# Optimization experiments

Measured on AMD Instinct MI355X. Metric: run time of the kernel, lower is better.

Reference implementation:

```python
import jax, jax.numpy as jnp
import numpy as np
from jax import lax

# NOTE: ResidualConvBlock and SS2DChanelFirst are reconstructed from the repo's
# conventions: ResidualConvBlock = act(conv3x3 -> act -> conv3x3 + 1x1 skip);
# SS2DChanelFirst = standard VMamba SS2D (in_proj -> dw-conv3x3 -> SiLU ->
# 4-direction cross-scan selective scan -> cross-merge -> LayerNorm -> *SiLU(z)
# gate -> out_proj) operating on NCHW tensors.

B, CIN, H, W = 4, 6, 64, 64
DM, DI, K, N, R, NL, GROUPS = 72, 144, 4, 8, 4, 2, 12


def conv2d(x, w, b=None, groups=1):
    out = lax.conv_general_dilated(x, w, (1, 1), 'SAME',
                                   dimension_numbers=('NCHW', 'OIHW', 'NCHW'),
                                   feature_group_count=groups)
    if b is not None:
        out = out + b[None, :, None, None]
    return out


def lrelu(x, s):
    return jnp.where(x >= 0, x, s * x)


def selective_scan(u, delta, A, Bs, Cs, D):
    # u, delta: (b,K,C,L); A: (K,C,N); Bs, Cs: (b,K,N,L); D: (K,C)
    b, k, c, l = u.shape
    n = A.shape[-1]
    ul = jnp.moveaxis(u, -1, 0)
    dl = jnp.moveaxis(delta, -1, 0)
    Bl = jnp.moveaxis(Bs, -1, 0)
    Cl = jnp.moveaxis(Cs, -1, 0)
    h0 = jnp.zeros((b, k, c, n), u.dtype)

    def step(h, xt):
        d_t, u_t, B_t, C_t = xt
        h = h * jnp.exp(d_t[..., None] * A) + (d_t * u_t)[..., None] * B_t[:, :, None, :]
        return h, jnp.einsum('bkcn,bkn->bkc', h, C_t)

    _, ys = lax.scan(step, h0, (dl, ul, Bl, Cl))
    return jnp.moveaxis(ys, 0, -1) + u * D[None, :, :, None]


def ss2d(x, in_w, dw_w, dw_b, xp_w, dtp_w, dtp_b, A_logs, Ds, ong, onb, op_w):
    b, dm, h_, w_ = x.shape
    l = h_ * w_
    xz = jnp.einsum('ec,bchw->behw', in_w, x)  # (b, 2*DI, h, w)
    xi, z = xz[:, :DI], xz[:, DI:]
    xi = jax.nn.silu(conv2d(xi, dw_w, dw_b, groups=DI))
    # cross-scan: row-major, col-major, and their reverses
    x0 = xi.reshape(b, DI, l)
    x1 = jnp.swapaxes(xi, 2, 3).reshape(b, DI, l)
    xs = jnp.stack([x0, x1, x0[..., ::-1], x1[..., ::-1]], axis=1)  # (b,4,DI,l)
    x_dbl = jnp.einsum('bkdl,kcd->bkcl', xs, xp_w)  # (b,4,R+2N,l)
    dts, Bs, Cs = x_dbl[:, :, :R], x_dbl[:, :, R:R + N], x_dbl[:, :, R + N:]
    dts = jnp.einsum('bkrl,kdr->bkdl', dts, dtp_w)
    delta = jax.nn.softplus(dts + dtp_b[None, :, :, None])
    A = -jnp.exp(A_logs).reshape(K, DI, N)
    ys = selective_scan(xs, delta, A, Bs, Cs, Ds.reshape(K, DI))  # (b,4,DI,l)
    # cross-merge
    y = ys[:, 0] + ys[:, 2, :, ::-1]
    yt = ys[:, 1] + ys[:, 3, :, ::-1]
    y = y + jnp.swapaxes(yt.reshape(b, DI, w_, h_), 2, 3).reshape(b, DI, l)
    y = jnp.swapaxes(y, 1, 2)  # (b,l,DI)
    mu = y.mean(-1, keepdims=True)
    var = ((y - mu) ** 2).mean(-1, keepdims=True)
    y = (y - mu) / jnp.sqrt(var + 1e-5) * ong + onb
    y = y * jax.nn.silu(jnp.swapaxes(z.reshape(b, DI, l), 1, 2))
    out = jnp.einsum('bld,ed->ble', y, op_w)  # (b,l,DM)
    return jnp.swapaxes(out, 1, 2).reshape(b, dm, h_, w_)


def groupnorm(x, g, bta, groups):
    b, c, h_, w_ = x.shape
    xg = x.reshape(b, groups, c // groups, h_ * w_)
    mu = xg.mean((2, 3), keepdims=True)
    var = ((xg - mu) ** 2).mean((2, 3), keepdims=True)
    xg = (xg - mu) / jnp.sqrt(var + 1e-5)
    return xg.reshape(b, c, h_, w_) * g[None, :, None, None] + bta[None, :, None, None]


def setup_inputs() -> dict:
    key = jax.random.key(0)
    ks = iter(jax.random.split(key, 32))
    nrm = lambda shp, s=0.05: jax.random.normal(next(ks), shp, jnp.float32) * s
    inp = {
        'image': jax.random.normal(next(ks), (B, CIN, H, W), jnp.float32),
        'cb_w1': nrm((DM, CIN, 3, 3), 0.1), 'cb_b1': nrm((DM,), 0.02),
        'cb_w2': nrm((DM, DM, 3, 3), 0.05), 'cb_b2': nrm((DM,), 0.02),
        'cb_ws': nrm((DM, CIN, 1, 1), 0.1), 'cb_bs': nrm((DM,), 0.02),
        'in_w': nrm((NL, 2 * DI, DM), 0.05),
        'dw_w': nrm((NL, DI, 1, 3, 3), 0.1), 'dw_b': nrm((NL, DI), 0.02),
        'xp_w': nrm((NL, K, R + 2 * N, DI), 0.05),
        'dtp_w': nrm((NL, K, DI, R), 0.1), 'dtp_b': nrm((NL, K, DI), 0.1),
        'A_logs': nrm((NL, K * DI, N), 0.5),
        'Ds': jnp.ones((NL, K * DI), jnp.float32) + nrm((NL, K * DI), 0.05),
        'ong': jnp.ones((NL, DI), jnp.float32), 'onb': jnp.zeros((NL, DI), jnp.float32),
        'op_w': nrm((NL, DM, DI), 0.05),
        'gn_g': jnp.ones((NL, DM), jnp.float32), 'gn_b': jnp.zeros((NL, DM), jnp.float32),
        'l1_w': nrm((NL, DM, DM), 0.1), 'l1_b': nrm((NL, DM), 0.02),
        'l2_w': nrm((NL, DM, DM), 0.1), 'l2_b': nrm((NL, DM), 0.02),
        'shrink_w': nrm((CIN, DM, 3, 3), 0.05), 'shrink_b': nrm((CIN,), 0.02),
    }
    return inp


def reference(image, cb_w1, cb_b1, cb_w2, cb_b2, cb_ws, cb_bs, in_w, dw_w, dw_b,
              xp_w, dtp_w, dtp_b, A_logs, Ds, ong, onb, op_w, gn_g, gn_b,
              l1_w, l1_b, l2_w, l2_b, shrink_w, shrink_b):
    # ResidualConvBlock (expand 6 -> 72), leaky_relu
    h = lrelu(conv2d(image, cb_w1, cb_b1), 0.01)
    h = conv2d(h, cb_w2, cb_b2) + conv2d(image, cb_ws, cb_bs)
    x = lrelu(h, 0.01)
    for i in range(NL):
        x = ss2d(x, in_w[i], dw_w[i], dw_b[i], xp_w[i], dtp_w[i], dtp_b[i],
                 A_logs[i], Ds[i], ong[i], onb[i], op_w[i])
        x = groupnorm(x, gn_g[i], gn_b[i], GROUPS)
        x = jnp.einsum('oc,bchw->bohw', l1_w[i], x) + l1_b[i][None, :, None, None]
        x = lrelu(x, 0.04)
        x = jnp.einsum('oc,bchw->bohw', l2_w[i], x) + l2_b[i][None, :, None, None]
    x = conv2d(x, shrink_w, shrink_b)
    return jax.nn.sigmoid(x)
```

## Files before the change

kernel.cpp:

```cpp
#include <hip/hip_runtime.h>
#include <math.h>

#define BB 4
#define CI 6
#define LL 4096
#define DMC 72
#define DIC 144
#define KD 4
#define NS 8
#define RD 4
#define NLAYER 2
#define GRP 12
#define NCH 128
#define TS 32
#define PP 4356
#define L2E 1.4426950408889634f

__device__ __forceinline__ float sigmoidf_(float x){ return 1.f/(1.f+__expf(-x)); }
__device__ __forceinline__ float siluf_(float x){ return x*sigmoidf_(x); }
__device__ __forceinline__ float softplusf_(float x){
  return fmaxf(x,0.f) + __logf(1.f + __expf(-fabsf(x)));
}

__device__ __forceinline__ int padidx(int p){ return 66*(p>>6) + (p&63) + 67; }

__device__ __forceinline__ int dirmap(int k, int l){
  switch(k & 3){
    case 0: return l;
    case 1: return ((l & 63) << 6) | (l >> 6);
    case 2: return (LL-1) - l;
    default: { int m = (LL-1) - l; return ((m & 63) << 6) | (m >> 6); }
  }
}

#define LOAD9(ip, a) do { \
  a[0]=(ip)[-67]; a[1]=(ip)[-66]; a[2]=(ip)[-65]; \
  a[3]=(ip)[-1];  a[4]=(ip)[0];   a[5]=(ip)[1];   \
  a[6]=(ip)[65];  a[7]=(ip)[66];  a[8]=(ip)[67];  } while(0)

__global__ void k_halo(float* __restrict__ pads, int nplanes){
  int plane = blockIdx.x;
  if (plane >= nplanes) return;
  int t = threadIdx.x;
  if (t >= 260) return;
  float* pl = pads + (size_t)plane*PP;
  int off;
  if (t < 132){
    int row = (t < 66) ? 0 : 65;
    int col = (t < 66) ? t : t-66;
    off = row*66 + col;
  } else {
    int j = t - 132;
    int col = (j < 64) ? 0 : 65;
    int row = 1 + (j & 63);
    off = row*66 + col;
  }
  pl[off] = 0.f;
}

__global__ void k_pad_img(const float* __restrict__ img, float* __restrict__ img_pad){
  int idx = blockIdx.x*256 + threadIdx.x;
  if (idx >= BB*CI*LL) return;
  int p = idx & 4095; int bc = idx >> 12;
  img_pad[(size_t)bc*PP + padidx(p)] = img[idx];
}

__global__ void k_conv1(const float* __restrict__ img_pad, const float* __restrict__ w,
                        const float* __restrict__ bias, float* __restrict__ tmp_pad){
  int bid = blockIdx.x;
  int t = bid & 15; int r = bid >> 4; int o = r % DMC; int b = r / DMC;
  int p = t*256 + threadIdx.x;
  int pb = padidx(p);
  float acc = bias[o];
  const float* wb = w + o*CI*9;
  #pragma unroll
  for (int ic=0; ic<CI; ++ic){
    const float* ip = img_pad + (size_t)(b*CI+ic)*PP + pb;
    float a[9]; LOAD9(ip, a);
    #pragma unroll
    for (int q=0;q<9;++q) acc += a[q]*wb[ic*9+q];
  }
  tmp_pad[(size_t)(b*DMC+o)*PP + pb] = acc >= 0.f ? acc : 0.01f*acc;
}

__global__ void k_conv2init(const float* __restrict__ img, const float* __restrict__ b2,
                            const float* __restrict__ wsc, const float* __restrict__ bsc,
                            float* __restrict__ xout){
  int bid = blockIdx.x;
  int t = bid & 15; int r = bid >> 4; int og = r % 18; int b = r / 18;
  int p = t*256 + threadIdx.x;
  float acc[4];
  #pragma unroll
  for (int j=0;j<4;++j) acc[j] = b2[og*4+j] + bsc[og*4+j];
  #pragma unroll
  for (int ic=0; ic<CI; ++ic){
    float v = img[((b*CI+ic)<<12)+p];
    #pragma unroll
    for (int j=0;j<4;++j) acc[j] += v * wsc[(og*4+j)*CI+ic];
  }
  #pragma unroll
  for (int j=0;j<4;++j)
    xout[((b*DMC+og*4+j)<<12)+p] = acc[j];
}

__global__ void k_conv2(const float* __restrict__ tmp_pad,
                        const float* __restrict__ w2, float* __restrict__ xout){
  int bid = blockIdx.x;
  int t = bid & 15; int r = bid >> 4; int og = r % 18; r /= 18;
  int icg = r & 1; int b = r >> 1;
  int p = t*256 + threadIdx.x;
  int pb = padidx(p);
  float acc[4] = {0.f,0.f,0.f,0.f};
  const float* ipb = tmp_pad + (size_t)b*DMC*PP + pb;
  const float* wb  = w2 + (size_t)(og*4)*DMC*9;
  #pragma unroll 2
  for (int ii=0; ii<36; ++ii){
    int ic = icg*36 + ii;
    const float* ip = ipb + (size_t)ic*PP;
    float a[9]; LOAD9(ip, a);
    const float* wp = wb + ic*9;
    #pragma unroll
    for (int j=0;j<4;++j){
      float s = 0.f;
      #pragma unroll
      for (int q=0;q<9;++q) s += a[q]*wp[(size_t)j*DMC*9 + q];
      acc[j] += s;
    }
  }
  #pragma unroll
  for (int j=0;j<4;++j)
    atomicAdd(xout + ((b*DMC+og*4+j)<<12)+p, acc[j]);
}

__global__ void k_xz(const float* __restrict__ x, const float* __restrict__ inw,
                     float* __restrict__ xz_pad, float* __restrict__ z_t, int relu){
  int bid = blockIdx.x;
  int t = bid & 15; int r = bid >> 4; int eg = r % 36; int b = r / 36;
  int p = t*256 + threadIdx.x;
  float acc[8] = {0.f,0.f,0.f,0.f,0.f,0.f,0.f,0.f};
  for (int c0=0; c0<DMC; c0+=4){
    float a[4];
    #pragma unroll
    for (int q=0;q<4;++q) a[q] = x[((b*DMC+c0+q)<<12)+p];
    if (relu){
      #pragma unroll
      for (int q=0;q<4;++q) a[q] = a[q] >= 0.f ? a[q] : 0.01f*a[q];
    }
    #pragma unroll
    for (int j=0;j<8;++j){
      float4 w = *(const float4*)(inw + (eg*8+j)*DMC + c0);
      acc[j] += a[0]*w.x + a[1]*w.y + a[2]*w.z + a[3]*w.w;
    }
  }
  if (eg < 18){
    int pb = padidx(p);
    #pragma unroll
    for (int j=0;j<8;++j) xz_pad[(size_t)(b*DIC+eg*8+j)*PP + pb] = acc[j];
  } else {
    float* zb = z_t + ((size_t)b*LL+p)*DIC + (eg*8-DIC);
    *(float4*)(zb)   = make_float4(acc[0],acc[1],acc[2],acc[3]);
    *(float4*)(zb+4) = make_float4(acc[4],acc[5],acc[6],acc[7]);
  }
}

__global__ void k_dw(const float* __restrict__ xz_pad, const float* __restrict__ dww,
                     const float* __restrict__ dwb, float* __restrict__ xi_t){
  int bid = blockIdx.x;
  int t = bid & 15; int r = bid >> 4; int c = r % DIC; int b = r / DIC;
  int p = t*256 + threadIdx.x;
  int pb = padidx(p);
  const float* ip = xz_pad + (size_t)(b*DIC+c)*PP + pb;
  const float* wp = dww + c*9;
  float a[9]; LOAD9(ip, a);
  float acc = dwb[c];
  #pragma unroll
  for (int q=0;q<9;++q) acc += a[q]*wp[q];
  xi_t[((size_t)b*LL+p)*DIC + c] = siluf_(acc);
}

__global__ void k_xdbl(const float* __restrict__ xi_t, const float* __restrict__ xpw,
                       float* __restrict__ xdbl){
  int bid = blockIdx.x;
  int t = bid & 15; int r = bid >> 4;
  int kk = r & 3; r >>= 2; int part = r % 10; int b = r / 10;
  int p = t*256 + threadIdx.x;
  const float* xib = xi_t + ((size_t)b*LL + p)*DIC;
  const float* wk = xpw + (size_t)(kk*20 + part*2)*DIC;
  float acc[2] = {0.f,0.f};
  for (int d=0; d<DIC; d+=4){
    float4 v = *(const float4*)(xib + d);
    #pragma unroll
    for (int c=0;c<2;++c){
      float4 w = *(const float4*)(wk + (size_t)c*DIC + d);
      acc[c] += v.x*w.x + v.y*w.y + v.z*w.z + v.w*w.w;
    }
  }
  float* dst = xdbl + ((size_t)(b*KD+kk)*LL + p)*20 + part*2;
  dst[0] = acc[0]; dst[1] = acc[1];
}

__device__ __forceinline__ void scan_decode(int idx, int& b, int& k, int& ch, int& c){
  c = idx % DIC;
  int r = idx / DIC;
  ch = r % NCH;
  r /= NCH;
  k = r & 3; b = r >> 2;
}

__global__ void k_p1(const float* __restrict__ xi_t, const float* __restrict__ xdbl,
                     const float* __restrict__ dtpw, const float* __restrict__ dtpb,
                     const float* __restrict__ alog,
                     float* __restrict__ cumA, float* __restrict__ hp){
  int idx = blockIdx.x*256 + threadIdx.x;
  if (idx >= BB*KD*NCH*DIC) return;
  int b,k,ch,c; scan_decode(idx,b,k,ch,c);
  float Arow[NS];
  #pragma unroll
  for (int n=0;n<NS;++n) Arow[n] = -__expf(alog[(k*DIC+c)*NS+n]) * L2E;
  float4 wdt = *(const float4*)(dtpw + (k*DIC+c)*RD);
  float bdt = dtpb[k*DIC+c];
  const float* xd = xdbl + (size_t)(b*KD+k)*LL*20;
  const float* xib = xi_t + (size_t)b*LL*DIC + c;
  float h[NS];
  #pragma unroll
  for (int n=0;n<NS;++n) h[n]=0.f;
  float sumd = 0.f;
  #pragma unroll 2
  for (int t=0; t<TS; ++t){
    int l = ch*TS + t;
    int ps = dirmap(k,l);
    const float* row = xd + (size_t)ps*20;
    float4 q0 = *(const float4*)(row);
    float4 q1 = *(const float4*)(row+4);
    float4 q2 = *(const float4*)(row+8);
    float u = xib[(size_t)ps*DIC];
    float dt = bdt + q0.x*wdt.x + q0.y*wdt.y + q0.z*wdt.z + q0.w*wdt.w;
    dt = softplusf_(dt);
    sumd += dt;
    float du = dt*u;
    float Bv[NS] = {q1.x,q1.y,q1.z,q1.w,q2.x,q2.y,q2.z,q2.w};
    #pragma unroll
    for (int n=0;n<NS;++n)
      h[n] = h[n]*exp2f(dt*Arow[n]) + du*Bv[n];
  }
  size_t base = ((size_t)((b*KD+k)*NCH + ch)*NS)*DIC + c;
  #pragma unroll
  for (int n=0;n<NS;++n) hp[base + n*DIC] = h[n];
  #pragma unroll
  for (int n=0;n<NS;++n) cumA[base + n*DIC] = exp2f(sumd*Arow[n]);
}

__global__ void k_p2(const float* __restrict__ cumA, float* __restrict__ hp){
  int idx = blockIdx.x*256 + threadIdx.x;
  if (idx >= BB*KD*NS*DIC) return;
  int c = idx % DIC; int n = (idx/DIC) % NS; int bk = idx/(DIC*NS);
  float h = 0.f;
  #pragma unroll 4
  for (int ch=0; ch<NCH; ++ch){
    size_t base = ((size_t)(bk*NCH+ch)*NS + n)*DIC + c;
    float a = cumA[base];
    float pp = hp[base];
    hp[base] = h;
    h = a*h + pp;
  }
}

__global__ void k_p3(const float* __restrict__ xi_t, const float* __restrict__ xdbl,
                     const float* __restrict__ dtpw, const float* __restrict__ dtpb,
                     const float* __restrict__ alog, const float* __restrict__ Dsv,
                     const float* __restrict__ hin, float* __restrict__ y_t){
  int idx = blockIdx.x*256 + threadIdx.x;
  if (idx >= BB*KD*NCH*DIC) return;
  int b,k,ch,c; scan_decode(idx,b,k,ch,c);
  float Arow[NS];
  #pragma unroll
  for (int n=0;n<NS;++n) Arow[n] = -__expf(alog[(k*DIC+c)*NS+n]) * L2E;
  float4 wdt = *(const float4*)(dtpw + (k*DIC+c)*RD);
  float bdt = dtpb[k*DIC+c];
  float Dv = Dsv[k*DIC+c];
  const float* xd = xdbl + (size_t)(b*KD+k)*LL*20;
  const float* xib = xi_t + (size_t)b*LL*DIC + c;
  float* yb = y_t + (size_t)b*LL*DIC + c;
  float h[NS];
  size_t base = ((size_t)((b*KD+k)*NCH + ch)*NS)*DIC + c;
  #pragma unroll
  for (int n=0;n<NS;++n) h[n] = hin[base + n*DIC];
  #pragma unroll 2
  for (int t=0; t<TS; ++t){
    int l = ch*TS + t;
    int ps = dirmap(k,l);
    const float* row = xd + (size_t)ps*20;
    float4 q0 = *(const float4*)(row);
    float4 q1 = *(const float4*)(row+4);
    float4 q2 = *(const float4*)(row+8);
    float4 q3 = *(const float4*)(row+12);
    float4 q4 = *(const float4*)(row+16);
    float u = xib[(size_t)ps*DIC];
    float dt = bdt + q0.x*wdt.x + q0.y*wdt.y + q0.z*wdt.z + q0.w*wdt.w;
    dt = softplusf_(dt);
    float du = dt*u;
    float Bv[NS] = {q1.x,q1.y,q1.z,q1.w,q2.x,q2.y,q2.z,q2.w};
    float Cv[NS] = {q3.x,q3.y,q3.z,q3.w,q4.x,q4.y,q4.z,q4.w};
    float y = 0.f;
    #pragma unroll
    for (int n=0;n<NS;++n){
      h[n] = h[n]*exp2f(dt*Arow[n]) + du*Bv[n];
      y += h[n]*Cv[n];
    }
    y += u*Dv;
    atomicAdd(yb + (size_t)ps*DIC, y);
  }
}

__global__ void k_oproj(const float* __restrict__ y_t, const float* __restrict__ z_t,
                        const float* __restrict__ ong, const float* __restrict__ onb,
                        const float* __restrict__ opw, float* __restrict__ xout){
  __shared__ float ly[DIC*65];
  __shared__ float red1[8][64], red2[8][64];
  __shared__ float lmu[64], lrs[64];
  int bid = blockIdx.x;
  int tile = bid & 63; int b = bid >> 6;
  int pstart = tile*64;
  const float* src = y_t + ((size_t)b*LL + pstart)*DIC;
  for (int i = threadIdx.x; i < 64*DIC; i += 512){
    int px = i / DIC; int d = i - px*DIC;
    ly[d*65 + px] = src[i];
  }
  __syncthreads();
  int px = threadIdx.x & 63;
  int grp = threadIdx.x >> 6;
  {
    float s=0.f, q=0.f;
    for (int d=grp*18; d<grp*18+18; ++d){
      float v = ly[d*65+px]; s += v; q += v*v;
    }
    red1[grp][px]=s; red2[grp][px]=q;
  }
  __syncthreads();
  if (grp == 0){
    float st=0.f, qt=0.f;
    #pragma unroll
    for (int g=0;g<8;++g){ st += red1[g][px]; qt += red2[g][px]; }
    float mu = st*(1.f/DIC);
    float var = qt*(1.f/DIC) - mu*mu;
    lmu[px] = mu;
    lrs[px] = rsqrtf(var + 1e-5f);
  }
  __syncthreads();
  const float* zsrc = z_t + ((size_t)b*LL + pstart)*DIC;
  for (int i = threadIdx.x; i < 64*DIC; i += 512){
    int ppx = i / DIC; int d = i - ppx*DIC;
    float zv = zsrc[i];
    float v = ly[d*65+ppx];
    ly[d*65+ppx] = ((v - lmu[ppx])*lrs[ppx]*ong[d] + onb[d]) * siluf_(zv);
  }
  __syncthreads();
  int ocg = __builtin_amdgcn_readfirstlane(grp);
  float acc[9];
  #pragma unroll
  for (int j=0;j<9;++j) acc[j]=0.f;
  const float* wb = opw + (size_t)ocg*9*DIC;
  #pragma unroll 4
  for (int d=0; d<DIC; ++d){
    float a = ly[d*65 + px];
    #pragma unroll
    for (int j=0;j<9;++j) acc[j] += a * wb[(size_t)j*DIC + d];
  }
  #pragma unroll
  for (int j=0;j<9;++j)
    xout[((size_t)(b*DMC + ocg*9 + j)<<12) + pstart + px] = acc[j];
}

__global__ void k_gnA(const float* __restrict__ x, float* __restrict__ stats){
  __shared__ float s1[256], s2[256];
  int bid = blockIdx.x;
  int t = bid & 15; int r = bid >> 4; int gr = r % GRP; int b = r / GRP;
  float ls=0.f, lq=0.f;
  #pragma unroll
  for (int it=0; it<6; ++it){
    int i = t*1536 + it*256 + threadIdx.x;
    int c = gr*6 + (i>>12); int p = i & 4095;
    float v = x[((size_t)(b*DMC+c)<<12)+p];
    ls += v; lq += v*v;
  }
  s1[threadIdx.x]=ls; s2[threadIdx.x]=lq; __syncthreads();
  for (int s=128; s>0; s>>=1){
    if (threadIdx.x < s){ s1[threadIdx.x]+=s1[threadIdx.x+s]; s2[threadIdx.x]+=s2[threadIdx.x+s]; }
    __syncthreads();
  }
  if (threadIdx.x == 0){
    atomicAdd(stats + (b*GRP+gr)*2,     s1[0]);
    atomicAdd(stats + (b*GRP+gr)*2 + 1, s2[0]);
  }
}

__global__ void k_gnAB(const float* __restrict__ stats, const float* __restrict__ g,
                       const float* __restrict__ bta, float* __restrict__ gnab){
  int idx = blockIdx.x*256 + threadIdx.x;
  if (idx >= BB*DMC) return;
  int c = idx % DMC; int b = idx / DMC; int gr = c / 6;
  float s = stats[(b*GRP+gr)*2];
  float q = stats[(b*GRP+gr)*2 + 1];
  const float inv = 1.f/(6.f*LL);
  float mu = s*inv;
  float var = q*inv - mu*mu;
  float rs = rsqrtf(var + 1e-5f);
  float A = rs*g[c];
  gnab[idx] = A;
  gnab[BB*DMC + idx] = bta[c] - mu*A;
}

__global__ void k_dense1(const float* __restrict__ xin, const float* __restrict__ gnab,
                         const float* __restrict__ w, const float* __restrict__ bias,
                         float* __restrict__ xout){
  int bid = blockIdx.x;
  int t = bid & 15; int r = bid >> 4; int eg = r % 36; int b = r / 36;
  int p = t*256 + threadIdx.x;
  float acc[2] = { bias[eg*2], bias[eg*2+1] };
  const float* Aab = gnab + b*DMC;
  const float* Bab = gnab + BB*DMC + b*DMC;
  for (int c0=0; c0<DMC; c0+=4){
    float a[4];
    #pragma unroll
    for (int q=0;q<4;++q){
      float v = xin[((size_t)(b*DMC+c0+q)<<12)+p];
      a[q] = v*Aab[c0+q] + Bab[c0+q];
    }
    #pragma unroll
    for (int j=0;j<2;++j){
      float4 w0 = *(const float4*)(w + (eg*2+j)*DMC + c0);
      acc[j] += a[0]*w0.x + a[1]*w0.y + a[2]*w0.z + a[3]*w0.w;
    }
  }
  #pragma unroll
  for (int j=0;j<2;++j)
    xout[((size_t)(b*DMC+eg*2+j)<<12)+p] = acc[j];
}

__global__ void k_dense2(const float* __restrict__ xin, const float* __restrict__ w,
                         const float* __restrict__ bias, float* __restrict__ xout,
                         float* __restrict__ pad_out){
  int bid = blockIdx.x;
  int t = bid & 15; int r = bid >> 4; int eg = r % 36; int b = r / 36;
  int p = t*256 + threadIdx.x;
  float acc[2] = { bias[eg*2], bias[eg*2+1] };
  for (int c0=0; c0<DMC; c0+=4){
    float a[4];
    #pragma unroll
    for (int q=0;q<4;++q){
      float v = xin[((size_t)(b*DMC+c0+q)<<12)+p];
      a[q] = v >= 0.f ? v : 0.04f*v;
    }
    #pragma unroll
    for (int j=0;j<2;++j){
      float4 w0 = *(const float4*)(w + (eg*2+j)*DMC + c0);
      acc[j] += a[0]*w0.x + a[1]*w0.y + a[2]*w0.z + a[3]*w0.w;
    }
  }
  #pragma unroll
  for (int j=0;j<2;++j){
    xout[((size_t)(b*DMC+eg*2+j)<<12)+p] = acc[j];
    if (pad_out) pad_out[(size_t)(b*DMC+eg*2+j)*PP + padidx(p)] = acc[j];
  }
}

__global__ void k_shrinkA(const float* __restrict__ x_pad, const float* __restrict__ w,
                          float* __restrict__ pacc){
  int bid = blockIdx.x;
  int t = bid & 15; int r = bid >> 4; int icg = r % 24; int b = r / 24;
  int p = t*256 + threadIdx.x;
  int pb = padidx(p);
  float acc[6] = {0.f,0.f,0.f,0.f,0.f,0.f};
  const float* ipb = x_pad + (size_t)b*DMC*PP + pb;
  #pragma unroll
  for (int ii=0; ii<3; ++ii){
    int ic = icg*3 + ii;
    const float* ip = ipb + (size_t)ic*PP;
    float a[9]; LOAD9(ip, a);
    #pragma unroll
    for (int o=0;o<6;++o){
      const float* wp = w + (o*DMC+ic)*9;
      float s = 0.f;
      #pragma unroll
      for (int q=0;q<9;++q) s += a[q]*wp[q];
      acc[o] += s;
    }
  }
  #pragma unroll
  for (int o=0;o<6;++o)
    atomicAdd(pacc + ((size_t)(b*CI+o)<<12)+p, acc[o]);
}

__global__ void k_sig(const float* __restrict__ pacc, const float* __restrict__ bias,
                      float* __restrict__ out){
  int idx = blockIdx.x*256 + threadIdx.x;
  if (idx >= BB*CI*LL) return;
  int o = (idx>>12) % CI;
  out[idx] = sigmoidf_(pacc[idx] + bias[o]);
}

extern "C" void kernel_launch(void* const* d_in, const int* in_sizes, int n_in,
                              void* d_out, int out_size, void* d_ws, size_t ws_size,
                              hipStream_t stream){
  const float* image = (const float*)d_in[0];
  const float* cb_w1 = (const float*)d_in[1];
  const float* cb_b1 = (const float*)d_in[2];
  const float* cb_w2 = (const float*)d_in[3];
  const float* cb_b2 = (const float*)d_in[4];
  const float* cb_ws = (const float*)d_in[5];
  const float* cb_bs = (const float*)d_in[6];
  const float* in_w  = (const float*)d_in[7];
  const float* dw_w  = (const float*)d_in[8];
  const float* dw_b  = (const float*)d_in[9];
  const float* xp_w  = (const float*)d_in[10];
  const float* dtp_w = (const float*)d_in[11];
  const float* dtp_b = (const float*)d_in[12];
  const float* A_logs= (const float*)d_in[13];
  const float* Ds    = (const float*)d_in[14];
  const float* ong   = (const float*)d_in[15];
  const float* onb   = (const float*)d_in[16];
  const float* op_w  = (const float*)d_in[17];
  const float* gn_g  = (const float*)d_in[18];
  const float* gn_b  = (const float*)d_in[19];
  const float* l1_w  = (const float*)d_in[20];
  const float* l1_b  = (const float*)d_in[21];
  const float* l2_w  = (const float*)d_in[22];
  const float* l2_b  = (const float*)d_in[23];
  const float* sh_w  = (const float*)d_in[24];
  const float* sh_b  = (const float*)d_in[25];

  const size_t SZ_X  = (size_t)BB*DMC*LL;
  const size_t SZ_C  = (size_t)BB*DIC*LL;
  const size_t SZ_XD = (size_t)BB*KD*20*LL;
  const size_t SZ_IP = (size_t)BB*CI*PP;
  const size_t SZ_TP = (size_t)BB*DMC*PP;
  const size_t SZ_ZP = (size_t)BB*DIC*PP;

  float* ws = (float*)d_ws;
  size_t off = 0;
  float* x     = ws + off; off += SZ_X;
  float* tmp   = ws + off; off += SZ_X;
  float* z_t   = ws + off; off += SZ_C;
  float* xi_t  = ws + off; off += SZ_C;
  float* xdbl  = ws + off; off += SZ_XD;
  float* cumA  = ws + off; off += SZ_C;
  float* hp    = ws + off; off += SZ_C;
  float* pads  = ws + off;
  float* img_pad = pads;
  float* tmp_pad = img_pad + SZ_IP;
  float* xz_pad  = tmp_pad + SZ_TP;
  off += SZ_IP + SZ_TP + SZ_ZP;
  float* gnstats = ws + off; off += 2*BB*GRP;
  float* gnab    = ws + off; off += 2*BB*DMC;
  if (ws_size < off*sizeof(float)) return;
  float* y_t = cumA;

  dim3 blk(256);
  const int NPLANES = BB*CI + BB*DMC + BB*DIC;

  k_halo<<<dim3(NPLANES), blk, 0, stream>>>(pads, NPLANES);
  k_pad_img<<<dim3(BB*CI*16), blk, 0, stream>>>(image, img_pad);
  k_conv1<<<dim3(BB*DMC*16), blk, 0, stream>>>(img_pad, cb_w1, cb_b1, tmp_pad);
  k_conv2init<<<dim3(BB*18*16), blk, 0, stream>>>(image, cb_b2, cb_ws, cb_bs, x);
  k_conv2<<<dim3(BB*2*18*16), blk, 0, stream>>>(tmp_pad, cb_w2, x);

  for (int i=0; i<NLAYER; ++i){
    const float* in_w_i  = in_w  + (size_t)i*2*DIC*DMC;
    const float* dw_w_i  = dw_w  + (size_t)i*DIC*9;
    const float* dw_b_i  = dw_b  + (size_t)i*DIC;
    const float* xp_w_i  = xp_w  + (size_t)i*KD*20*DIC;
    const float* dtp_w_i = dtp_w + (size_t)i*KD*DIC*RD;
    const float* dtp_b_i = dtp_b + (size_t)i*KD*DIC;
    const float* alog_i  = A_logs+ (size_t)i*KD*DIC*NS;
    const float* Ds_i    = Ds    + (size_t)i*KD*DIC;
    const float* ong_i   = ong   + (size_t)i*DIC;
    const float* onb_i   = onb   + (size_t)i*DIC;
    const float* op_w_i  = op_w  + (size_t)i*DMC*DIC;
    const float* gn_g_i  = gn_g  + (size_t)i*DMC;
    const float* gn_b_i  = gn_b  + (size_t)i*DMC;
    const float* l1_w_i  = l1_w  + (size_t)i*DMC*DMC;
    const float* l1_b_i  = l1_b  + (size_t)i*DMC;
    const float* l2_w_i  = l2_w  + (size_t)i*DMC*DMC;
    const float* l2_b_i  = l2_b  + (size_t)i*DMC;

    k_xz  <<<dim3(BB*36*16), blk, 0, stream>>>(x, in_w_i, xz_pad, z_t, (i==0)?1:0);
    k_dw  <<<dim3(BB*DIC*16), blk, 0, stream>>>(xz_pad, dw_w_i, dw_b_i, xi_t);
    k_xdbl<<<dim3(BB*10*KD*16), blk, 0, stream>>>(xi_t, xp_w_i, xdbl);
    k_p1  <<<dim3(BB*KD*NCH*DIC/256), blk, 0, stream>>>(xi_t, xdbl, dtp_w_i, dtp_b_i, alog_i, cumA, hp);
    k_p2  <<<dim3(BB*KD*NS*DIC/256), blk, 0, stream>>>(cumA, hp);
    hipMemsetAsync(y_t, 0, SZ_C*sizeof(float), stream);
    k_p3  <<<dim3(BB*KD*NCH*DIC/256), blk, 0, stream>>>(xi_t, xdbl, dtp_w_i, dtp_b_i, alog_i, Ds_i, hp, y_t);
    k_oproj<<<dim3(BB*64), dim3(512), 0, stream>>>(y_t, z_t, ong_i, onb_i, op_w_i, x);
    hipMemsetAsync(gnstats, 0, 2*BB*GRP*sizeof(float), stream);
    k_gnA <<<dim3(BB*GRP*16), blk, 0, stream>>>(x, gnstats);
    k_gnAB<<<dim3(2), blk, 0, stream>>>(gnstats, gn_g_i, gn_b_i, gnab);
    k_dense1<<<dim3(BB*36*16), blk, 0, stream>>>(x, gnab, l1_w_i, l1_b_i, tmp);
    k_dense2<<<dim3(BB*36*16), blk, 0, stream>>>(tmp, l2_w_i, l2_b_i, x,
                                                 (i==NLAYER-1) ? tmp_pad : (float*)nullptr);
  }

  hipMemsetAsync(tmp, 0, (size_t)BB*CI*LL*sizeof(float), stream);
  k_shrinkA<<<dim3(BB*24*16), blk, 0, stream>>>(tmp_pad, sh_w, tmp);
  k_sig<<<dim3((BB*CI*LL+255)/256), blk, 0, stream>>>(tmp, sh_b, (float*)d_out);
}
```

Measured before the change: 538.8 us.

## Double scan chunk count, widen per-thread outputs, and fold memsets into kernels

The chunked selective scan now uses 256 chunks of 16 steps instead of 128 of 32, with deeper unrolling, to expose more parallel threads in the first and third scan passes. The x_dbl projection and both dense 1x1 layers compute more output channels per thread, cutting the number of blocks and the repeated input reads. The two memsets are removed: the second scan pass zeroes the cumA buffer that is reused as y_t, and the output-projection kernel zeroes the group-norm stats. The scan carry buffers grow to match the larger chunk count, and the extra chunks make the sequential second pass longer.

```diff
diff --git a/kernel.cpp b/kernel.cpp
--- a/kernel.cpp
+++ b/kernel.cpp
@@ -11,8 +11,8 @@
 #define RD 4
 #define NLAYER 2
 #define GRP 12
-#define NCH 128
-#define TS 32
+#define NCH 256
+#define TS 16
 #define PP 4356
 #define L2E 1.4426950408889634f
 
@@ -182,21 +182,22 @@
                        float* __restrict__ xdbl){
   int bid = blockIdx.x;
   int t = bid & 15; int r = bid >> 4;
-  int kk = r & 3; r >>= 2; int part = r % 10; int b = r / 10;
+  int kk = r & 3; r >>= 2; int part = r & 3; int b = r >> 2;
   int p = t*256 + threadIdx.x;
   const float* xib = xi_t + ((size_t)b*LL + p)*DIC;
-  const float* wk = xpw + (size_t)(kk*20 + part*2)*DIC;
-  float acc[2] = {0.f,0.f};
+  const float* wk = xpw + (size_t)(kk*20 + part*5)*DIC;
+  float acc[5] = {0.f,0.f,0.f,0.f,0.f};
   for (int d=0; d<DIC; d+=4){
     float4 v = *(const float4*)(xib + d);
     #pragma unroll
-    for (int c=0;c<2;++c){
+    for (int c=0;c<5;++c){
       float4 w = *(const float4*)(wk + (size_t)c*DIC + d);
       acc[c] += v.x*w.x + v.y*w.y + v.z*w.z + v.w*w.w;
     }
   }
-  float* dst = xdbl + ((size_t)(b*KD+kk)*LL + p)*20 + part*2;
-  dst[0] = acc[0]; dst[1] = acc[1];
+  float* dst = xdbl + ((size_t)(b*KD+kk)*LL + p)*20 + part*5;
+  #pragma unroll
+  for (int c=0;c<5;++c) dst[c] = acc[c];
 }
 
 __device__ __forceinline__ void scan_decode(int idx, int& b, int& k, int& ch, int& c){
@@ -225,7 +226,7 @@
   #pragma unroll
   for (int n=0;n<NS;++n) h[n]=0.f;
   float sumd = 0.f;
-  #pragma unroll 2
+  #pragma unroll 4
   for (int t=0; t<TS; ++t){
     int l = ch*TS + t;
     int ps = dirmap(k,l);
@@ -250,7 +251,7 @@
   for (int n=0;n<NS;++n) cumA[base + n*DIC] = exp2f(sumd*Arow[n]);
 }
 
-__global__ void k_p2(const float* __restrict__ cumA, float* __restrict__ hp){
+__global__ void k_p2(float* __restrict__ cumA, float* __restrict__ hp){
   int idx = blockIdx.x*256 + threadIdx.x;
   if (idx >= BB*KD*NS*DIC) return;
   int c = idx % DIC; int n = (idx/DIC) % NS; int bk = idx/(DIC*NS);
@@ -260,6 +261,7 @@
     size_t base = ((size_t)(bk*NCH+ch)*NS + n)*DIC + c;
     float a = cumA[base];
     float pp = hp[base];
+    cumA[base] = 0.f;
     hp[base] = h;
     h = a*h + pp;
   }
@@ -285,7 +287,7 @@
   size_t base = ((size_t)((b*KD+k)*NCH + ch)*NS)*DIC + c;
   #pragma unroll
   for (int n=0;n<NS;++n) h[n] = hin[base + n*DIC];
-  #pragma unroll 2
+  #pragma unroll 4
   for (int t=0; t<TS; ++t){
     int l = ch*TS + t;
     int ps = dirmap(k,l);
@@ -314,11 +316,13 @@
 
 __global__ void k_oproj(const float* __restrict__ y_t, const float* __restrict__ z_t,
                         const float* __restrict__ ong, const float* __restrict__ onb,
-                        const float* __restrict__ opw, float* __restrict__ xout){
+                        const float* __restrict__ opw, float* __restrict__ xout,
+                        float* __restrict__ gnstats){
   __shared__ float ly[DIC*65];
   __shared__ float red1[8][64], red2[8][64];
   __shared__ float lmu[64], lrs[64];
   int bid = blockIdx.x;
+  if (bid == 0 && threadIdx.x < 2*BB*GRP) gnstats[threadIdx.x] = 0.f;
   int tile = bid & 63; int b = bid >> 6;
   int pstart = tile*64;
   const float* src = y_t + ((size_t)b*LL + pstart)*DIC;
@@ -414,9 +418,11 @@
                          const float* __restrict__ w, const float* __restrict__ bias,
                          float* __restrict__ xout){
   int bid = blockIdx.x;
-  int t = bid & 15; int r = bid >> 4; int eg = r % 36; int b = r / 36;
-  int p = t*256 + threadIdx.x;
-  float acc[2] = { bias[eg*2], bias[eg*2+1] };
+  int t = bid & 15; int r = bid >> 4; int eg = r % 18; int b = r / 18;
+  int p = t*256 + threadIdx.x;
+  float acc[4];
+  #pragma unroll
+  for (int j=0;j<4;++j) acc[j] = bias[eg*4+j];
   const float* Aab = gnab + b*DMC;
   const float* Bab = gnab + BB*DMC + b*DMC;
   for (int c0=0; c0<DMC; c0+=4){
@@ -427,23 +433,25 @@
       a[q] = v*Aab[c0+q] + Bab[c0+q];
     }
     #pragma unroll
-    for (int j=0;j<2;++j){
-      float4 w0 = *(const float4*)(w + (eg*2+j)*DMC + c0);
+    for (int j=0;j<4;++j){
+      float4 w0 = *(const float4*)(w + (eg*4+j)*DMC + c0);
       acc[j] += a[0]*w0.x + a[1]*w0.y + a[2]*w0.z + a[3]*w0.w;
     }
   }
   #pragma unroll
-  for (int j=0;j<2;++j)
-    xout[((size_t)(b*DMC+eg*2+j)<<12)+p] = acc[j];
+  for (int j=0;j<4;++j)
+    xout[((size_t)(b*DMC+eg*4+j)<<12)+p] = acc[j];
 }
 
 __global__ void k_dense2(const float* __restrict__ xin, const float* __restrict__ w,
                          const float* __restrict__ bias, float* __restrict__ xout,
                          float* __restrict__ pad_out){
   int bid = blockIdx.x;
-  int t = bid & 15; int r = bid >> 4; int eg = r % 36; int b = r / 36;
-  int p = t*256 + threadIdx.x;
-  float acc[2] = { bias[eg*2], bias[eg*2+1] };
+  int t = bid & 15; int r = bid >> 4; int eg = r % 18; int b = r / 18;
+  int p = t*256 + threadIdx.x;
+  float acc[4];
+  #pragma unroll
+  for (int j=0;j<4;++j) acc[j] = bias[eg*4+j];
   for (int c0=0; c0<DMC; c0+=4){
     float a[4];
     #pragma unroll
@@ -452,15 +460,16 @@
       a[q] = v >= 0.f ? v : 0.04f*v;
     }
     #pragma unroll
-    for (int j=0;j<2;++j){
-      float4 w0 = *(const float4*)(w + (eg*2+j)*DMC + c0);
+    for (int j=0;j<4;++j){
+      float4 w0 = *(const float4*)(w + (eg*4+j)*DMC + c0);
       acc[j] += a[0]*w0.x + a[1]*w0.y + a[2]*w0.z + a[3]*w0.w;
     }
   }
-  #pragma unroll
-  for (int j=0;j<2;++j){
-    xout[((size_t)(b*DMC+eg*2+j)<<12)+p] = acc[j];
-    if (pad_out) pad_out[(size_t)(b*DMC+eg*2+j)*PP + padidx(p)] = acc[j];
+  int pb = padidx(p);
+  #pragma unroll
+  for (int j=0;j<4;++j){
+    xout[((size_t)(b*DMC+eg*4+j)<<12)+p] = acc[j];
+    if (pad_out) pad_out[(size_t)(b*DMC+eg*4+j)*PP + pb] = acc[j];
   }
 }
 
@@ -532,6 +541,7 @@
   const size_t SZ_X  = (size_t)BB*DMC*LL;
   const size_t SZ_C  = (size_t)BB*DIC*LL;
   const size_t SZ_XD = (size_t)BB*KD*20*LL;
+  const size_t SZ_HP = (size_t)BB*KD*NCH*NS*DIC;
   const size_t SZ_IP = (size_t)BB*CI*PP;
   const size_t SZ_TP = (size_t)BB*DMC*PP;
   const size_t SZ_ZP = (size_t)BB*DIC*PP;
@@ -543,8 +553,8 @@
   float* z_t   = ws + off; off += SZ_C;
   float* xi_t  = ws + off; off += SZ_C;
   float* xdbl  = ws + off; off += SZ_XD;
-  float* cumA  = ws + off; off += SZ_C;
-  float* hp    = ws + off; off += SZ_C;
+  float* cumA  = ws + off; off += SZ_HP;
+  float* hp    = ws + off; off += SZ_HP;
   float* pads  = ws + off;
   float* img_pad = pads;
   float* tmp_pad = img_pad + SZ_IP;
@@ -585,17 +595,15 @@
 
     k_xz  <<<dim3(BB*36*16), blk, 0, stream>>>(x, in_w_i, xz_pad, z_t, (i==0)?1:0);
     k_dw  <<<dim3(BB*DIC*16), blk, 0, stream>>>(xz_pad, dw_w_i, dw_b_i, xi_t);
-    k_xdbl<<<dim3(BB*10*KD*16), blk, 0, stream>>>(xi_t, xp_w_i, xdbl);
+    k_xdbl<<<dim3(BB*4*KD*16), blk, 0, stream>>>(xi_t, xp_w_i, xdbl);
     k_p1  <<<dim3(BB*KD*NCH*DIC/256), blk, 0, stream>>>(xi_t, xdbl, dtp_w_i, dtp_b_i, alog_i, cumA, hp);
     k_p2  <<<dim3(BB*KD*NS*DIC/256), blk, 0, stream>>>(cumA, hp);
-    hipMemsetAsync(y_t, 0, SZ_C*sizeof(float), stream);
     k_p3  <<<dim3(BB*KD*NCH*DIC/256), blk, 0, stream>>>(xi_t, xdbl, dtp_w_i, dtp_b_i, alog_i, Ds_i, hp, y_t);
-    k_oproj<<<dim3(BB*64), dim3(512), 0, stream>>>(y_t, z_t, ong_i, onb_i, op_w_i, x);
-    hipMemsetAsync(gnstats, 0, 2*BB*GRP*sizeof(float), stream);
+    k_oproj<<<dim3(BB*64), dim3(512), 0, stream>>>(y_t, z_t, ong_i, onb_i, op_w_i, x, gnstats);
     k_gnA <<<dim3(BB*GRP*16), blk, 0, stream>>>(x, gnstats);
     k_gnAB<<<dim3(2), blk, 0, stream>>>(gnstats, gn_g_i, gn_b_i, gnab);
-    k_dense1<<<dim3(BB*36*16), blk, 0, stream>>>(x, gnab, l1_w_i, l1_b_i, tmp);
-    k_dense2<<<dim3(BB*36*16), blk, 0, stream>>>(tmp, l2_w_i, l2_b_i, x,
+    k_dense1<<<dim3(BB*18*16), blk, 0, stream>>>(x, gnab, l1_w_i, l1_b_i, tmp);
+    k_dense2<<<dim3(BB*18*16), blk, 0, stream>>>(tmp, l2_w_i, l2_b_i, x,
                                                  (i==NLAYER-1) ? tmp_pad : (float*)nullptr);
   }
 
```

Result: faster. 502.1 us (-6.8%).
